# Performance work log

Measured on AMD Instinct MI355X. Metric: run time of the kernel, lower is better.

The kernel has to match this reference:

```python
import jax, jax.numpy as jnp
import numpy as np

ALPHA = 0.25
GAMMA = 2.0
EPS = 1e-8
W_CLASS = 2.0
W_BBOX = 5.0
W_GIOU = 2.0
PROB_THRESH = 0.5
BBOX_THRESH = -0.1
BIG = 1e9  # cost assigned to filtered-out (masked) pseudo targets


def box_cxcywh_to_xyxy(b):
    cx, cy, w, h = b[..., 0], b[..., 1], b[..., 2], b[..., 3]
    return jnp.stack([cx - 0.5 * w, cy - 0.5 * h, cx + 0.5 * w, cy + 0.5 * h], axis=-1)


def generalized_box_iou(boxes1, boxes2):
    # boxes1: [..., N, 4] xyxy, boxes2: [..., M, 4] xyxy -> [..., N, M]
    area1 = (boxes1[..., 2] - boxes1[..., 0]) * (boxes1[..., 3] - boxes1[..., 1])
    area2 = (boxes2[..., 2] - boxes2[..., 0]) * (boxes2[..., 3] - boxes2[..., 1])
    lt = jnp.maximum(boxes1[..., :, None, :2], boxes2[..., None, :, :2])
    rb = jnp.minimum(boxes1[..., :, None, 2:], boxes2[..., None, :, 2:])
    wh = jnp.clip(rb - lt, 0.0)
    inter = wh[..., 0] * wh[..., 1]
    union = area1[..., :, None] + area2[..., None, :] - inter
    iou = inter / union
    lt_c = jnp.minimum(boxes1[..., :, None, :2], boxes2[..., None, :, :2])
    rb_c = jnp.maximum(boxes1[..., :, None, 2:], boxes2[..., None, :, 2:])
    wh_c = jnp.clip(rb_c - lt_c, 0.0)
    area_c = wh_c[..., 0] * wh_c[..., 1]
    return iou - (area_c - union) / area_c


def setup_inputs() -> dict:
    key = jax.random.key(0)
    k1, k2, k3, k4, k5 = jax.random.split(key, 5)
    B, Q, C, T = 32, 900, 91, 30
    return {
        "pred_logits": jax.random.normal(k1, (B, Q, C), dtype=jnp.float32),
        "pred_boxes": jax.random.uniform(k2, (B, Q, 4), dtype=jnp.float32),
        "pred_logits_base": jax.random.normal(k3, (B, Q, C), dtype=jnp.float32),
        "pred_boxes_base": jax.random.uniform(k4, (B, Q, 4), dtype=jnp.float32),
        "targets_boxes": jax.random.uniform(k5, (B, T, 4), dtype=jnp.float32),
    }


def reference(pred_logits, pred_boxes, pred_logits_base, pred_boxes_base, targets_boxes):
    # ---- pseudo-label generation from the base model (original: sort + python filter) ----
    prob_base = jax.nn.sigmoid(pred_logits_base)          # [B, Qb, C]
    top_prob = jnp.max(prob_base, axis=-1)                # [B, Qb]
    pseudo_labels = jnp.argmax(prob_base, axis=-1)        # [B, Qb] (idx_base[..., 0])
    keep_prob = top_prob > PROB_THRESH
    # original per-box loop: keep if all(-giou(pseudo, gt) > bbox_thresh)
    g_pt = generalized_box_iou(box_cxcywh_to_xyxy(pred_boxes_base),
                               box_cxcywh_to_xyxy(targets_boxes))  # [B, Qb, T]
    keep_giou = jnp.all(-g_pt > BBOX_THRESH, axis=-1)     # [B, Qb]
    pseudo_mask = keep_prob & keep_giou                   # valid pseudo-target slots

    # ---- cost matrix between current predictions and pseudo targets ----
    out_prob = jax.nn.sigmoid(pred_logits)                # [B, Q, C]
    # gather class prob at each pseudo target's label: [B, Q, Qb]
    p = jnp.take_along_axis(out_prob, pseudo_labels[:, None, :], axis=2)
    pos_cost = ALPHA * (1.0 - p) ** GAMMA * (-jnp.log(p + EPS))
    neg_cost = (1.0 - ALPHA) * p ** GAMMA * (-jnp.log(1.0 - p + EPS))
    cost_class = pos_cost - neg_cost

    # L1 cdist between cxcywh boxes: [B, Q, Qb]
    cost_bbox = jnp.sum(jnp.abs(pred_boxes[:, :, None, :] - pred_boxes_base[:, None, :, :]), axis=-1)

    cost_giou = -generalized_box_iou(box_cxcywh_to_xyxy(pred_boxes),
                                     box_cxcywh_to_xyxy(pred_boxes_base))  # [B, Q, Qb]

    C = W_BBOX * cost_bbox + W_CLASS * cost_class + W_GIOU * cost_giou
    # masked (filtered-out) pseudo targets get a huge cost so they are never matched
    C = jnp.where(pseudo_mask[:, None, :], C, BIG)
    return C, pseudo_mask
```

## Files before the change

kernel.cpp:

```cpp
#include <hip/hip_runtime.h>

static constexpr int B  = 32;
static constexpr int Q  = 900;
static constexpr int NC = 91;
static constexpr int T  = 30;
static constexpr int QT = 18;

static constexpr float ALPHA_  = 0.25f;
static constexpr float EPS_    = 1e-8f;
static constexpr float W_CLASS = 2.0f;
static constexpr float W_BBOX  = 5.0f;
static constexpr float W_GIOU  = 2.0f;
static constexpr float BIG_    = 1e9f;

__global__ __launch_bounds__(256) void k1_mask_label(
    const float* __restrict__ logits_base,
    const float4* __restrict__ boxes_base,
    const float4* __restrict__ targets,
    int* __restrict__ labels,
    float* __restrict__ mask_out) {
#pragma clang fp contract(off)
  int wid  = (blockIdx.x * blockDim.x + threadIdx.x) >> 6;
  int lane = threadIdx.x & 63;
  if (wid >= B * Q) return;
  int b = wid / Q;

  const float* row = logits_base + (size_t)wid * NC;
  float v  = (lane < NC) ? row[lane] : -1e30f;
  int  arg = lane;
  int lane2 = lane + 64;
  if (lane2 < NC) {
    float v2 = row[lane2];
    if (v2 > v) { v = v2; arg = lane2; }
  }
  for (int off = 32; off >= 1; off >>= 1) {
    float ov = __shfl_xor(v, off, 64);
    int   oi = __shfl_xor(arg, off, 64);
    if (ov > v || (ov == v && oi < arg)) { v = ov; arg = oi; }
  }
  bool keep = (v > 0.0f);

  float4 bb = boxes_base[wid];
  float x1 = bb.x - 0.5f * bb.z, y1 = bb.y - 0.5f * bb.w;
  float x2 = bb.x + 0.5f * bb.z, y2 = bb.y + 0.5f * bb.w;
  float a1 = (x2 - x1) * (y2 - y1);

  bool ok = true;
  if (lane < T) {
    float4 tb = targets[b * T + lane];
    float tx1 = tb.x - 0.5f * tb.z, ty1 = tb.y - 0.5f * tb.w;
    float tx2 = tb.x + 0.5f * tb.z, ty2 = tb.y + 0.5f * tb.w;
    float a2 = (tx2 - tx1) * (ty2 - ty1);
    float ltx = fmaxf(x1, tx1), lty = fmaxf(y1, ty1);
    float rbx = fminf(x2, tx2), rby = fminf(y2, ty2);
    float iw = fmaxf(rbx - ltx, 0.0f), ih = fmaxf(rby - lty, 0.0f);
    float inter = iw * ih;
    float uni = (a1 + a2) - inter;
    float iou = inter / uni;
    float cx1 = fminf(x1, tx1), cy1 = fminf(y1, ty1);
    float cx2 = fmaxf(x2, tx2), cy2 = fmaxf(y2, ty2);
    float cw = fmaxf(cx2 - cx1, 0.0f), ch = fmaxf(cy2 - cy1, 0.0f);
    float ac = cw * ch;
    float g = iou - (ac - uni) / ac;
    ok = (-g > -0.1f);
  }
  keep = keep && __all(ok);

  if (lane == 0) {
    labels[wid]   = arg;
    mask_out[wid] = keep ? 1.0f : 0.0f;
  }
}

__device__ __forceinline__ float class_cost(float x) {
  float p   = __builtin_amdgcn_rcpf(1.0f + __expf(-x));
  float omp = 1.0f - p;
  float pos = ALPHA_ * (omp * omp) * (-__logf(p + EPS_));
  float neg = (1.0f - ALPHA_) * (p * p) * (-__logf(omp + EPS_));
  return pos - neg;
}

__global__ __launch_bounds__(256) void k3_cost(
    const float* __restrict__ pred_logits,
    const float4* __restrict__ pred_boxes,
    const float4* __restrict__ boxes_base,
    const int* __restrict__ labels,
    const float* __restrict__ mask_in,
    float* __restrict__ Cout) {
  __shared__ float s_cc[QT * NC];
  __shared__ float s_row[QT][12];

  int b   = blockIdx.x / (Q / QT);
  int q0  = (blockIdx.x % (Q / QT)) * QT;
  int tid = threadIdx.x;

  const float* lg = pred_logits + ((size_t)(b * Q + q0)) * NC;
  for (int i = tid; i < QT * NC; i += 256) s_cc[i] = class_cost(lg[i]);

  if (tid < QT) {
    float4 pb = pred_boxes[b * Q + q0 + tid];
    float px1 = pb.x - 0.5f * pb.z, py1 = pb.y - 0.5f * pb.w;
    float px2 = pb.x + 0.5f * pb.z, py2 = pb.y + 0.5f * pb.w;
    s_row[tid][0] = pb.x; s_row[tid][1] = pb.y;
    s_row[tid][2] = pb.z; s_row[tid][3] = pb.w;
    s_row[tid][4] = px1;  s_row[tid][5] = py1;
    s_row[tid][6] = px2;  s_row[tid][7] = py2;
    s_row[tid][8] = (px2 - px1) * (py2 - py1);
  }

  bool active = (tid < Q / 4);
  float cxb[4], cyb[4], wbx[4], hbx[4], x1b[4], y1b[4], x2b[4], y2b[4], ab[4];
  int lb[4];
  bool mk[4];
  int jbase = b * Q + 4 * tid;
  if (active) {
    int4 lbv = *reinterpret_cast<const int4*>(labels + jbase);
    float4 mkv = *reinterpret_cast<const float4*>(mask_in + jbase);
    lb[0] = lbv.x; lb[1] = lbv.y; lb[2] = lbv.z; lb[3] = lbv.w;
    mk[0] = mkv.x != 0.0f; mk[1] = mkv.y != 0.0f;
    mk[2] = mkv.z != 0.0f; mk[3] = mkv.w != 0.0f;
#pragma unroll
    for (int k = 0; k < 4; ++k) {
      float4 bb = boxes_base[jbase + k];
      cxb[k] = bb.x; cyb[k] = bb.y; wbx[k] = bb.z; hbx[k] = bb.w;
      x1b[k] = bb.x - 0.5f * bb.z; y1b[k] = bb.y - 0.5f * bb.w;
      x2b[k] = bb.x + 0.5f * bb.z; y2b[k] = bb.y + 0.5f * bb.w;
      ab[k]  = (x2b[k] - x1b[k]) * (y2b[k] - y1b[k]);
    }
  }
  __syncthreads();

  if (active) {
    size_t rowbase = ((size_t)(b * Q + q0)) * Q;
    for (int qi = 0; qi < QT; ++qi, rowbase += Q) {
      float pcx = s_row[qi][0], pcy = s_row[qi][1];
      float pw  = s_row[qi][2], ph  = s_row[qi][3];
      float px1 = s_row[qi][4], py1 = s_row[qi][5];
      float px2 = s_row[qi][6], py2 = s_row[qi][7];
      float pa  = s_row[qi][8];
      const float* ccq = s_cc + qi * NC;
      float res[4];
#pragma unroll
      for (int k = 0; k < 4; ++k) {
        float cls = ccq[lb[k]];
        float l1 = fabsf(pcx - cxb[k]) + fabsf(pcy - cyb[k]) +
                   fabsf(pw - wbx[k]) + fabsf(ph - hbx[k]);
        float ltx = fmaxf(px1, x1b[k]), lty = fmaxf(py1, y1b[k]);
        float rbx = fminf(px2, x2b[k]), rby = fminf(py2, y2b[k]);
        float iw = fmaxf(rbx - ltx, 0.0f), ih = fmaxf(rby - lty, 0.0f);
        float inter = iw * ih;
        float uni = (pa + ab[k]) - inter;
        float iou = inter * __builtin_amdgcn_rcpf(uni);
        float c1x = fminf(px1, x1b[k]), c1y = fminf(py1, y1b[k]);
        float c2x = fmaxf(px2, x2b[k]), c2y = fmaxf(py2, y2b[k]);
        float cw = fmaxf(c2x - c1x, 0.0f), ch = fmaxf(c2y - c1y, 0.0f);
        float acl = cw * ch;
        float g = iou - (acl - uni) * __builtin_amdgcn_rcpf(acl);
        float cost = W_BBOX * l1 + W_CLASS * cls - W_GIOU * g;
        res[k] = mk[k] ? cost : BIG_;
      }
      float4 out4 = make_float4(res[0], res[1], res[2], res[3]);
      *reinterpret_cast<float4*>(Cout + rowbase + 4 * tid) = out4;
    }
  }
}

extern "C" void kernel_launch(void* const* d_in, const int* in_sizes, int n_in,
                              void* d_out, int out_size, void* d_ws, size_t ws_size,
                              hipStream_t stream) {
  const float*  pred_logits      = (const float*)d_in[0];
  const float4* pred_boxes       = (const float4*)d_in[1];
  const float*  pred_logits_base = (const float*)d_in[2];
  const float4* pred_boxes_base  = (const float4*)d_in[3];
  const float4* targets          = (const float4*)d_in[4];

  float* out      = (float*)d_out;
  float* mask_out = out + (size_t)B * Q * Q;

  int* labels = (int*)d_ws;

  k1_mask_label<<<(B * Q * 64) / 256, 256, 0, stream>>>(
      pred_logits_base, pred_boxes_base, targets, labels, mask_out);

  k3_cost<<<B * (Q / QT), 256, 0, stream>>>(
      pred_logits, pred_boxes, pred_boxes_base, labels, mask_out, out);
}
```

Before: 54.34 us.

## Precompute class cost in separate kernel, simplify GIoU math, shrink query tile

Moves the per-element focal class-cost evaluation out of the cost kernel into a standalone vectorized kernel that writes to workspace, so each cost-kernel block only copies precomputed values into shared memory. The GIoU inner loop is rewritten algebraically so the enclosing box comes from summed widths minus overlap, with a single reciprocal of uni*acl. The mask is folded into an additive constant instead of a select, and the query tile shrinks from 18 to 12 rows per block. This adds a kernel launch and an extra global round trip for the class-cost array, and the algebraic GIoU form can differ slightly in precision and in degenerate cases.

After: 49.86 us. -8.2%, faster.

```diff
diff --git a/kernel.cpp b/kernel.cpp
--- a/kernel.cpp
+++ b/kernel.cpp
@@ -4,13 +4,10 @@
 static constexpr int Q  = 900;
 static constexpr int NC = 91;
 static constexpr int T  = 30;
-static constexpr int QT = 18;
+static constexpr int QT = 12;
 
 static constexpr float ALPHA_  = 0.25f;
 static constexpr float EPS_    = 1e-8f;
-static constexpr float W_CLASS = 2.0f;
-static constexpr float W_BBOX  = 5.0f;
-static constexpr float W_GIOU  = 2.0f;
 static constexpr float BIG_    = 1e9f;
 
 __global__ __launch_bounds__(256) void k1_mask_label(
@@ -80,45 +77,62 @@
   return pos - neg;
 }
 
+__global__ __launch_bounds__(256) void k2_class_cost(
+    const float4* __restrict__ lg, float4* __restrict__ cc, int n4) {
+  int i = blockIdx.x * 256 + threadIdx.x;
+  if (i < n4) {
+    float4 v = lg[i];
+    float4 o;
+    o.x = class_cost(v.x);
+    o.y = class_cost(v.y);
+    o.z = class_cost(v.z);
+    o.w = class_cost(v.w);
+    cc[i] = o;
+  }
+}
+
 __global__ __launch_bounds__(256) void k3_cost(
-    const float* __restrict__ pred_logits,
+    const float* __restrict__ cc_all,
     const float4* __restrict__ pred_boxes,
     const float4* __restrict__ boxes_base,
     const int* __restrict__ labels,
     const float* __restrict__ mask_in,
     float* __restrict__ Cout) {
-  __shared__ float s_cc[QT * NC];
-  __shared__ float s_row[QT][12];
+  __shared__ float  s_cc[QT * NC];
+  __shared__ float4 s_row[QT][2];
+  __shared__ float  s_pa[QT];
 
   int b   = blockIdx.x / (Q / QT);
   int q0  = (blockIdx.x % (Q / QT)) * QT;
   int tid = threadIdx.x;
 
-  const float* lg = pred_logits + ((size_t)(b * Q + q0)) * NC;
-  for (int i = tid; i < QT * NC; i += 256) s_cc[i] = class_cost(lg[i]);
+  const float4* ccs = reinterpret_cast<const float4*>(
+      cc_all + ((size_t)(b * Q + q0)) * NC);
+  float4* sc4 = reinterpret_cast<float4*>(s_cc);
+  for (int i = tid; i < QT * NC / 4; i += 256) sc4[i] = ccs[i];
 
   if (tid < QT) {
     float4 pb = pred_boxes[b * Q + q0 + tid];
     float px1 = pb.x - 0.5f * pb.z, py1 = pb.y - 0.5f * pb.w;
     float px2 = pb.x + 0.5f * pb.z, py2 = pb.y + 0.5f * pb.w;
-    s_row[tid][0] = pb.x; s_row[tid][1] = pb.y;
-    s_row[tid][2] = pb.z; s_row[tid][3] = pb.w;
-    s_row[tid][4] = px1;  s_row[tid][5] = py1;
-    s_row[tid][6] = px2;  s_row[tid][7] = py2;
-    s_row[tid][8] = (px2 - px1) * (py2 - py1);
+    s_row[tid][0] = pb;
+    s_row[tid][1] = make_float4(px1, py1, px2, py2);
+    s_pa[tid] = (px2 - px1) * (py2 - py1);
   }
 
   bool active = (tid < Q / 4);
   float cxb[4], cyb[4], wbx[4], hbx[4], x1b[4], y1b[4], x2b[4], y2b[4], ab[4];
+  float c2big[4];
   int lb[4];
-  bool mk[4];
   int jbase = b * Q + 4 * tid;
   if (active) {
     int4 lbv = *reinterpret_cast<const int4*>(labels + jbase);
     float4 mkv = *reinterpret_cast<const float4*>(mask_in + jbase);
     lb[0] = lbv.x; lb[1] = lbv.y; lb[2] = lbv.z; lb[3] = lbv.w;
-    mk[0] = mkv.x != 0.0f; mk[1] = mkv.y != 0.0f;
-    mk[2] = mkv.z != 0.0f; mk[3] = mkv.w != 0.0f;
+    c2big[0] = 2.0f + (mkv.x != 0.0f ? 0.0f : BIG_);
+    c2big[1] = 2.0f + (mkv.y != 0.0f ? 0.0f : BIG_);
+    c2big[2] = 2.0f + (mkv.z != 0.0f ? 0.0f : BIG_);
+    c2big[3] = 2.0f + (mkv.w != 0.0f ? 0.0f : BIG_);
 #pragma unroll
     for (int k = 0; k < 4; ++k) {
       float4 bb = boxes_base[jbase + k];
@@ -131,36 +145,33 @@
   __syncthreads();
 
   if (active) {
-    size_t rowbase = ((size_t)(b * Q + q0)) * Q;
+    size_t rowbase = ((size_t)(b * Q + q0)) * Q + 4 * tid;
+#pragma unroll
     for (int qi = 0; qi < QT; ++qi, rowbase += Q) {
-      float pcx = s_row[qi][0], pcy = s_row[qi][1];
-      float pw  = s_row[qi][2], ph  = s_row[qi][3];
-      float px1 = s_row[qi][4], py1 = s_row[qi][5];
-      float px2 = s_row[qi][6], py2 = s_row[qi][7];
-      float pa  = s_row[qi][8];
+      float4 pc = s_row[qi][0];
+      float4 pe = s_row[qi][1];
+      float pa  = s_pa[qi];
       const float* ccq = s_cc + qi * NC;
       float res[4];
 #pragma unroll
       for (int k = 0; k < 4; ++k) {
         float cls = ccq[lb[k]];
-        float l1 = fabsf(pcx - cxb[k]) + fabsf(pcy - cyb[k]) +
-                   fabsf(pw - wbx[k]) + fabsf(ph - hbx[k]);
-        float ltx = fmaxf(px1, x1b[k]), lty = fmaxf(py1, y1b[k]);
-        float rbx = fminf(px2, x2b[k]), rby = fminf(py2, y2b[k]);
-        float iw = fmaxf(rbx - ltx, 0.0f), ih = fmaxf(rby - lty, 0.0f);
+        float l1 = fabsf(pc.x - cxb[k]) + fabsf(pc.y - cyb[k]) +
+                   fabsf(pc.z - wbx[k]) + fabsf(pc.w - hbx[k]);
+        float mwx = fminf(pe.z, x2b[k]) - fmaxf(pe.x, x1b[k]);
+        float mwy = fminf(pe.w, y2b[k]) - fmaxf(pe.y, y1b[k]);
+        float iw = fmaxf(mwx, 0.0f), ih = fmaxf(mwy, 0.0f);
         float inter = iw * ih;
         float uni = (pa + ab[k]) - inter;
-        float iou = inter * __builtin_amdgcn_rcpf(uni);
-        float c1x = fminf(px1, x1b[k]), c1y = fminf(py1, y1b[k]);
-        float c2x = fmaxf(px2, x2b[k]), c2y = fmaxf(py2, y2b[k]);
-        float cw = fmaxf(c2x - c1x, 0.0f), ch = fmaxf(c2y - c1y, 0.0f);
+        float cw = (pc.z + wbx[k]) - mwx;
+        float ch = (pc.w + hbx[k]) - mwy;
         float acl = cw * ch;
-        float g = iou - (acl - uni) * __builtin_amdgcn_rcpf(acl);
-        float cost = W_BBOX * l1 + W_CLASS * cls - W_GIOU * g;
-        res[k] = mk[k] ? cost : BIG_;
+        float r = __builtin_amdgcn_rcpf(uni * acl);
+        float t = (inter * acl + uni * uni) * r;
+        res[k] = fmaf(-2.0f, t, fmaf(5.0f, l1, fmaf(2.0f, cls, c2big[k])));
       }
-      float4 out4 = make_float4(res[0], res[1], res[2], res[3]);
-      *reinterpret_cast<float4*>(Cout + rowbase + 4 * tid) = out4;
+      *reinterpret_cast<float4*>(Cout + rowbase) =
+          make_float4(res[0], res[1], res[2], res[3]);
     }
   }
 }
@@ -177,11 +188,16 @@
   float* out      = (float*)d_out;
   float* mask_out = out + (size_t)B * Q * Q;
 
-  int* labels = (int*)d_ws;
+  int*   labels = (int*)d_ws;
+  float* cc     = (float*)((char*)d_ws + 131072);
 
   k1_mask_label<<<(B * Q * 64) / 256, 256, 0, stream>>>(
       pred_logits_base, pred_boxes_base, targets, labels, mask_out);
 
+  int n4 = B * Q * NC / 4;
+  k2_class_cost<<<(n4 + 255) / 256, 256, 0, stream>>>(
+      (const float4*)pred_logits, (float4*)cc, n4);
+
   k3_cost<<<B * (Q / QT), 256, 0, stream>>>(
-      pred_logits, pred_boxes, pred_boxes_base, labels, mask_out, out);
-}
+      cc, pred_boxes, pred_boxes_base, labels, mask_out, out);
+}
```
